# Optimization experiments

Measured on AMD Instinct MI355X. Metric: run time of the kernel, lower is better.

The kernel has to match this reference:

```python
import jax, jax.numpy as jnp
import numpy as np

B, N, C = 16, 4096, 512
PW, PH = 64, 64  # N = PW * PH
POOL = 2         # attention_pool_scale
D_SCALE = 1.0 / float(np.sqrt(C))


def setup_inputs() -> dict:
    key = jax.random.key(0)
    ks = jax.random.split(key, 4)
    w_std = 1.0 / float(np.sqrt(C))
    return {
        "x": jax.random.normal(ks[0], (B, N, C), dtype=jnp.float32),
        "Wq": jax.random.normal(ks[1], (C, C), dtype=jnp.float32) * w_std,
        "bq": jnp.zeros((C,), dtype=jnp.float32),
        "Wk": jax.random.normal(ks[2], (C, C), dtype=jnp.float32) * w_std,
        "bk": jnp.zeros((C,), dtype=jnp.float32),
        "Wv": jax.random.normal(ks[3], (C, C), dtype=jnp.float32) * w_std,
        "bv": jnp.zeros((C,), dtype=jnp.float32),
    }


def _to_spatial(t):
    # [B, N, C] -> [B, C, PW, PH]
    return t.transpose(0, 2, 1).reshape(t.shape[0], C, PW, PH)


def reference(x, Wq, bq, Wk, bk, Wv, bv):
    # Linear (torch convention y = x @ W^T + b) + sigmoid activation
    def proj(W, b):
        return jax.nn.sigmoid(jnp.einsum('bnc,dc->bnd', x, W) + b)

    Q = _to_spatial(proj(Wq, bq))  # [B, C, PW, PH]
    K = _to_spatial(proj(Wk, bk))
    V = _to_spatial(proj(Wv, bv))

    # avg_pool2d with kernel (POOL, 1): pool over PW axis
    q = Q.reshape(B, C, PW // POOL, POOL, PH).mean(axis=3)  # [B, C, PW/2, PH]
    k = K.reshape(B, C, PW // POOL, POOL, PH).mean(axis=3)

    # Qk = softmax(scale * Q @ k^T): [B, C, PW, PW/2]
    Qk = jax.nn.softmax(D_SCALE * jnp.einsum('bcik,bcjk->bcij', Q, k), axis=-1)
    # Kq = softmax(scale * q @ K^T): [B, C, PW/2, PW]
    Kq = jax.nn.softmax(D_SCALE * jnp.einsum('bcik,bcjk->bcij', q, K), axis=-1)
    # Kqv = Kq @ V: [B, C, PW/2, PH]
    Kqv = jnp.einsum('bcij,bcjk->bcik', Kq, V)
    # out = Qk @ Kqv: [B, C, PW, PH]
    out = jnp.einsum('bcij,bcjk->bcik', Qk, Kqv)

    # spatial -> sequence: [B, C, PW*PH] -> [B, N, C]
    return out.reshape(B, C, N).transpose(0, 2, 1)
```

## Files before the change

kernel.cpp:

```cpp
#include <hip/hip_runtime.h>
#include <hip/hip_bf16.h>
#include <string.h>

typedef __hip_bfloat16  bf16;
typedef __hip_bfloat162 bf162;
typedef __attribute__((ext_vector_type(8))) short short8;
typedef __attribute__((ext_vector_type(4))) float f32x4;

#define NB 16
#define NN 4096
#define NC 512
#define SCALE 0.044194173824159216f

#define GLL16(gp, lp) __builtin_amdgcn_global_load_lds( \
    (__attribute__((address_space(1))) void*)(gp),      \
    (__attribute__((address_space(3))) void*)(lp), 16, 0, 0)

__global__ __launch_bounds__(256) void cast_x_kernel(
    const float* __restrict__ x, bf16* __restrict__ xb)
{
    size_t i = ((size_t)blockIdx.x * 256 + threadIdx.x) * 8;
    float4 a = *(const float4*)(x + i);
    float4 b = *(const float4*)(x + i + 4);
    bf16 t[8];
    t[0] = __float2bfloat16(a.x); t[1] = __float2bfloat16(a.y);
    t[2] = __float2bfloat16(a.z); t[3] = __float2bfloat16(a.w);
    t[4] = __float2bfloat16(b.x); t[5] = __float2bfloat16(b.y);
    t[6] = __float2bfloat16(b.z); t[7] = __float2bfloat16(b.w);
    uint4 r; memcpy(&r, t, 16);
    *(uint4*)(xb + i) = r;
}

__global__ __launch_bounds__(256) void cast_w_kernel(
    const float* __restrict__ Wq, const float* __restrict__ Wk,
    const float* __restrict__ Wv, bf16* __restrict__ Wb)
{
    const float* W = (blockIdx.y == 0) ? Wq : (blockIdx.y == 1) ? Wk : Wv;
    size_t i = ((size_t)blockIdx.x * 256 + threadIdx.x) * 8;
    float4 a = *(const float4*)(W + i);
    float4 b = *(const float4*)(W + i + 4);
    bf16 t[8];
    t[0] = __float2bfloat16(a.x); t[1] = __float2bfloat16(a.y);
    t[2] = __float2bfloat16(a.z); t[3] = __float2bfloat16(a.w);
    t[4] = __float2bfloat16(b.x); t[5] = __float2bfloat16(b.y);
    t[6] = __float2bfloat16(b.z); t[7] = __float2bfloat16(b.w);
    uint4 r; memcpy(&r, t, 16);
    *(uint4*)(Wb + (size_t)blockIdx.y * (NC * NC) + i) = r;
}

__global__ __launch_bounds__(256) void proj_mfma(
    const bf16* __restrict__ xb, const bf16* __restrict__ Wb,
    const float* __restrict__ bq, const float* __restrict__ bk,
    const float* __restrict__ bv,
    bf16* __restrict__ Qs, bf16* __restrict__ Ks, bf16* __restrict__ Vs)
{
    __shared__ __align__(16) char smem[36864];
    short* As = (short*)smem;
    short* Bs = (short*)(smem + 16384);
    bf16*  OutS = (bf16*)smem;

    const int tid = threadIdx.x;
    const int w   = tid >> 6;
    const int l   = tid & 63;
    const int q   = l >> 4;
    const int mrow= l & 15;
    const int wr  = w >> 1;
    const int wc  = w & 1;

    const int bx = blockIdx.x;
    const int m  = bx >> 2;
    const int d0 = (bx & 3) * 128;
    const int r0 = blockIdx.y * 128;
    const int b  = r0 >> 12;
    const int n0 = r0 & 4095;

    const bf16*  W    = Wb + (size_t)m * (NC * NC);
    const float* bias = (m == 0) ? bq : (m == 1) ? bk : bv;
    bf16*        Out  = (m == 0) ? Qs : (m == 1) ? Ks : Vs;

    f32x4 acc[4][4];
    const f32x4 z = {0.f, 0.f, 0.f, 0.f};
    #pragma unroll
    for (int i = 0; i < 4; ++i)
        #pragma unroll
        for (int j = 0; j < 4; ++j) acc[i][j] = z;

    const int srow = tid >> 3;
    const int scol = (tid & 7) * 8;
    const int sxor = ((tid ^ (tid >> 3)) & 7) * 8;
    const int axor = (mrow & 7) * 8;

    for (int k0 = 0; k0 < NC; k0 += 64) {
        #pragma unroll
        for (int c = 0; c < 4; ++c) {
            int row = srow + 32 * c;
            GLL16(xb + (size_t)(r0 + row) * NC + k0 + sxor, &As[row * 64 + scol]);
        }
        #pragma unroll
        for (int c = 0; c < 4; ++c) {
            int row = srow + 32 * c;
            GLL16(W + (size_t)(d0 + row) * NC + k0 + sxor, &Bs[row * 64 + scol]);
        }
        __syncthreads();

        #pragma unroll
        for (int ks = 0; ks < 2; ++ks) {
            short8 af[4], bfr[4];
            #pragma unroll
            for (int ti = 0; ti < 4; ++ti)
                af[ti] = *(const short8*)&As[(64 * wr + 16 * ti + mrow) * 64 +
                                             ((q * 8 + 32 * ks) ^ axor)];
            #pragma unroll
            for (int tj = 0; tj < 4; ++tj)
                bfr[tj] = *(const short8*)&Bs[(64 * wc + 16 * tj + mrow) * 64 +
                                              ((q * 8 + 32 * ks) ^ axor)];
            #pragma unroll
            for (int ti = 0; ti < 4; ++ti)
                #pragma unroll
                for (int tj = 0; tj < 4; ++tj)
                    acc[ti][tj] = __builtin_amdgcn_mfma_f32_16x16x32_bf16(
                        af[ti], bfr[tj], acc[ti][tj], 0, 0, 0);
        }
        __syncthreads();
    }

    float bb[4];
    #pragma unroll
    for (int tj = 0; tj < 4; ++tj) bb[tj] = bias[d0 + 64 * wc + 16 * tj + mrow];

    #pragma unroll
    for (int ti = 0; ti < 4; ++ti)
        #pragma unroll
        for (int tj = 0; tj < 4; ++tj) {
            int d = 64 * wc + 16 * tj + mrow;
            bf16 t4[4];
            #pragma unroll
            for (int g = 0; g < 4; ++g) {
                float v = acc[ti][tj][g] + bb[tj];
                t4[g] = __float2bfloat16(1.0f / (1.0f + __expf(-v)));
            }
            uint2 pk; memcpy(&pk, t4, 8);
            *(uint2*)&OutS[d * 144 + 64 * wr + 16 * ti + 4 * q] = pk;
        }
    __syncthreads();

    #pragma unroll
    for (int v = 0; v < 8; ++v) {
        int e  = tid + 256 * v;
        int d  = e >> 4;
        int ch = e & 15;
        uint4 r = *(const uint4*)&OutS[d * 144 + ch * 8];
        *(uint4*)(Out + ((size_t)b * NC + d0 + d) * NN + n0 + ch * 8) = r;
    }
}

__global__ __launch_bounds__(256) void attn_mfma(
    const bf16* __restrict__ Qs, const bf16* __restrict__ Ks,
    const bf16* __restrict__ Vs, bf16* __restrict__ Os)
{
    __shared__ __align__(16) char smem[24064];
    bf16* VT  = (bf16*)smem;
    bf16* S1b = (bf16*)(smem + 9216);
    bf16* S2b = (bf16*)(smem + 9216 + 5120);
    bf16* KVT = (bf16*)(smem + 9216 + 5120 + 4608);

    const int tid = threadIdx.x;
    const int w   = tid >> 6;
    const int l   = tid & 63;
    const int m   = l & 15;
    const int q   = l >> 4;
    const size_t base = (size_t)blockIdx.x * NN;

    uint4  vr[2];
    short8 aQ[2];
    short8 bK8[8];
    {
        const uint4* src = (const uint4*)(Vs + base);
        vr[0] = src[tid];
        vr[1] = src[tid + 256];
        #pragma unroll
        for (int ks = 0; ks < 2; ++ks)
            aQ[ks] = *(const short8*)(Qs + base + (16 * w + m) * 64 + q * 8 + 32 * ks);
        #pragma unroll
        for (int tj = 0; tj < 4; ++tj)
            #pragma unroll
            for (int ks = 0; ks < 2; ++ks)
                bK8[tj * 2 + ks] = *(const short8*)(Ks + base + (16 * tj + m) * 64 + q * 8 + 32 * ks);
    }

    {
        #pragma unroll
        for (int v = 0; v < 2; ++v) {
            int e = tid + 256 * v;
            bf16 tmp[8]; memcpy(tmp, &vr[v], 16);
            int pw = e >> 3;
            int a  = e & 7;
            int cs = (((pw >> 3) ^ a) & 7) << 3;
            int c7 = pw & 7;
            #pragma unroll
            for (int t = 0; t < 8; ++t)
                VT[(8 * a + t) * 72 + cs + c7] = tmp[t];
        }
    }

    f32x4 tacc[4];
    {
        const f32x4 z = {0.f, 0.f, 0.f, 0.f};
        __builtin_amdgcn_s_setprio(1);
        #pragma unroll
        for (int tj = 0; tj < 4; ++tj) {
            tacc[tj] = z;
            #pragma unroll
            for (int ks = 0; ks < 2; ++ks)
                tacc[tj] = __builtin_amdgcn_mfma_f32_16x16x32_bf16(
                    aQ[ks], bK8[tj * 2 + ks], tacc[tj], 0, 0, 0);
        }
        __builtin_amdgcn_s_setprio(0);
    }

    {
        float e[4][4], s[4] = {0.f, 0.f, 0.f, 0.f};
        #pragma unroll
        for (int t = 0; t < 4; ++t)
            #pragma unroll
            for (int r = 0; r < 4; ++r) {
                float v  = tacc[t][r];
                float pv = (v + __shfl_xor(v, 1)) * (0.5f * SCALE);
                e[t][r] = __expf(pv);
                s[r] += e[t][r];
            }
        #pragma unroll
        for (int r = 0; r < 4; ++r) {
            #pragma unroll
            for (int d = 1; d < 16; d <<= 1)
                s[r] += __shfl_xor(s[r], d);
            s[r] = 2.0f / s[r];
        }
        {
            int jc = m >> 1;
            int t0 = (l & 1) * 2;
            #pragma unroll
            for (int tt = 0; tt < 2; ++tt) {
                int t = t0 + tt;
                #pragma unroll
                for (int r = 0; r < 4; ++r)
                    S1b[(16 * w + q * 4 + r) * 40 + t * 8 + jc] =
                        __float2bfloat16(e[t][r] * s[r]);
            }
        }
    }

    {
        float e2[4][2], s2[2] = {0.f, 0.f};
        #pragma unroll
        for (int t = 0; t < 4; ++t)
            #pragma unroll
            for (int h = 0; h < 2; ++h) {
                float pv = (tacc[t][2 * h] + tacc[t][2 * h + 1]) * (0.5f * SCALE);
                e2[t][h] = __expf(pv);
                s2[h] += e2[t][h];
            }
        #pragma unroll
        for (int h = 0; h < 2; ++h) {
            #pragma unroll
            for (int d = 1; d < 16; d <<= 1)
                s2[h] += __shfl_xor(s2[h], d);
            s2[h] = 1.0f / s2[h];
        }
        #pragma unroll
        for (int t = 0; t < 4; ++t)
            #pragma unroll
            for (int h = 0; h < 2; ++h)
                S2b[(8 * w + q * 2 + h) * 72 + t * 16 + m] =
                    __float2bfloat16(e2[t][h] * s2[h]);
    }
    __syncthreads();

    {
        const int rb = (2 * w + (m >> 3)) & 7;
        short8 aV[2];
        #pragma unroll
        for (int ks = 0; ks < 2; ++ks)
            aV[ks] = *(const short8*)&VT[(16 * w + m) * 72 +
                                         (((q + 4 * ks) ^ rb) & 7) * 8];
        __builtin_amdgcn_s_setprio(1);
        #pragma unroll
        for (int tn = 0; tn < 2; ++tn) {
            f32x4 kacc = {0.f, 0.f, 0.f, 0.f};
            #pragma unroll
            for (int ks = 0; ks < 2; ++ks) {
                short8 bS = *(const short8*)&S2b[(16 * tn + m) * 72 + q * 8 + 32 * ks];
                kacc = __builtin_amdgcn_mfma_f32_16x16x32_bf16(bS, aV[ks], kacc, 0, 0, 0);
            }
            bf16 t4[4];
            #pragma unroll
            for (int r = 0; r < 4; ++r) t4[r] = __float2bfloat16(kacc[r]);
            uint2 pk; memcpy(&pk, t4, 8);
            *(uint2*)&KVT[(16 * w + m) * 40 + 16 * tn + 4 * q] = pk;
        }
        __builtin_amdgcn_s_setprio(0);
    }
    __syncthreads();

    {
        short8 aS = *(const short8*)&S1b[(16 * w + m) * 40 + q * 8];
        __builtin_amdgcn_s_setprio(1);
        #pragma unroll
        for (int tn = 0; tn < 4; ++tn) {
            short8 bKV = *(const short8*)&KVT[(16 * tn + m) * 40 + q * 8];
            f32x4 z = {0.f, 0.f, 0.f, 0.f};
            f32x4 oacc = __builtin_amdgcn_mfma_f32_16x16x32_bf16(aS, bKV, z, 0, 0, 0);
            bf16 t4[4];
            #pragma unroll
            for (int r = 0; r < 4; ++r) t4[r] = __float2bfloat16(oacc[r]);
            uint2 pk; memcpy(&pk, t4, 8);
            *(uint2*)(Os + base + (size_t)(16 * tn + m) * 64 + 16 * w + 4 * q) = pk;
        }
        __builtin_amdgcn_s_setprio(0);
    }
}

__global__ __launch_bounds__(256) void unspat_kernel(
    const bf16* __restrict__ Os, float* __restrict__ out)
{
    __shared__ float t[32][65];
    const int b  = blockIdx.z;
    const int c0 = blockIdx.y * 32;
    const int bx = blockIdx.x;
    const int a0 = bx * 64;
    const int tx = threadIdx.x & 31;
    const int ty = threadIdx.x >> 5;
    const bf162* src = (const bf162*)(Os + ((size_t)b * NC + c0) * NN + a0);
    #pragma unroll
    for (int r = 0; r < 4; ++r) {
        int cc = ty + r * 8;
        float2 f = __bfloat1622float2(src[(size_t)cc * (NN/2) + tx]);
        t[cc][2*tx] = f.x; t[cc][2*tx+1] = f.y;
    }
    __syncthreads();
    float* dstB = out + ((size_t)b * NN) * NC + c0;
    #pragma unroll
    for (int r = 0; r < 8; ++r) {
        int nn = ty + r * 8;
        dstB[(size_t)(nn * 64 + bx) * NC + tx] = t[tx][nn];
    }
}

extern "C" void kernel_launch(void* const* d_in, const int* in_sizes, int n_in,
                              void* d_out, int out_size, void* d_ws, size_t ws_size,
                              hipStream_t stream)
{
    const float* x  = (const float*)d_in[0];
    const float* Wq = (const float*)d_in[1];
    const float* bq = (const float*)d_in[2];
    const float* Wk = (const float*)d_in[3];
    const float* bk = (const float*)d_in[4];
    const float* Wv = (const float*)d_in[5];
    const float* bv = (const float*)d_in[6];
    float* out = (float*)d_out;

    const size_t S = (size_t)NB * NC * NN;
    bf16* Qb = (bf16*)d_ws;
    bf16* Kb = Qb + S;
    bf16* Vb = Kb + S;
    bf16* xb = (bf16*)d_out;
    bf16* Wb = ((bf16*)d_out) + S;

    cast_x_kernel<<<dim3((NB * NN * NC) / (256 * 8)), 256, 0, stream>>>(x, xb);
    cast_w_kernel<<<dim3((NC * NC) / (256 * 8), 3), 256, 0, stream>>>(Wq, Wk, Wv, Wb);
    proj_mfma<<<dim3(12, (NB * NN) / 128), 256, 0, stream>>>(
        xb, Wb, bq, bk, bv, Qb, Kb, Vb);
    attn_mfma<<<dim3(NB * NC), 256, 0, stream>>>(Qb, Kb, Vb, Qb);
    unspat_kernel<<<dim3(NN / 64, NC / 32, NB), 256, 0, stream>>>(Qb, out);
}
```

Measured before the change: 497.0 us.

## Remap projection grid for XCD-aware L2 reuse and load K fragments lazily in attention

The projection kernel now runs on a 1D grid and remaps each workgroup index so that consecutive groups on the same XCD (index mod 8) share the same 128-row x tile across all 12 weight/column slices. This is meant to improve L2 reuse of x and W on MI355X, whose chiplets have separate L2 caches. In the attention kernel, the K fragments are no longer preloaded into a register array and are instead loaded just before each MFMA. That lowers register pressure but can expose load latency right before the matrix ops.

```diff
diff --git a/kernel.cpp b/kernel.cpp
--- a/kernel.cpp
+++ b/kernel.cpp
@@ -67,10 +67,13 @@
     const int wr  = w >> 1;
     const int wc  = w & 1;
 
-    const int bx = blockIdx.x;
-    const int m  = bx >> 2;
-    const int d0 = (bx & 3) * 128;
-    const int r0 = blockIdx.y * 128;
+    const int wg = blockIdx.x;
+    const int i  = wg >> 3;
+    const int s  = i % 12;
+    const int r  = (wg & 7) * 64 + i / 12;
+    const int m  = s >> 2;
+    const int d0 = (s & 3) * 128;
+    const int r0 = r * 128;
     const int b  = r0 >> 12;
     const int n0 = r0 & 4095;
 
@@ -81,9 +84,9 @@
     f32x4 acc[4][4];
     const f32x4 z = {0.f, 0.f, 0.f, 0.f};
     #pragma unroll
-    for (int i = 0; i < 4; ++i)
-        #pragma unroll
-        for (int j = 0; j < 4; ++j) acc[i][j] = z;
+    for (int ii = 0; ii < 4; ++ii)
+        #pragma unroll
+        for (int j = 0; j < 4; ++j) acc[ii][j] = z;
 
     const int srow = tid >> 3;
     const int scol = (tid & 7) * 8;
@@ -149,8 +152,8 @@
         int e  = tid + 256 * v;
         int d  = e >> 4;
         int ch = e & 15;
-        uint4 r = *(const uint4*)&OutS[d * 144 + ch * 8];
-        *(uint4*)(Out + ((size_t)b * NC + d0 + d) * NN + n0 + ch * 8) = r;
+        uint4 rr = *(const uint4*)&OutS[d * 144 + ch * 8];
+        *(uint4*)(Out + ((size_t)b * NC + d0 + d) * NN + n0 + ch * 8) = rr;
     }
 }
 
@@ -173,7 +176,6 @@
 
     uint4  vr[2];
     short8 aQ[2];
-    short8 bK8[8];
     {
         const uint4* src = (const uint4*)(Vs + base);
         vr[0] = src[tid];
@@ -181,11 +183,6 @@
         #pragma unroll
         for (int ks = 0; ks < 2; ++ks)
             aQ[ks] = *(const short8*)(Qs + base + (16 * w + m) * 64 + q * 8 + 32 * ks);
-        #pragma unroll
-        for (int tj = 0; tj < 4; ++tj)
-            #pragma unroll
-            for (int ks = 0; ks < 2; ++ks)
-                bK8[tj * 2 + ks] = *(const short8*)(Ks + base + (16 * tj + m) * 64 + q * 8 + 32 * ks);
     }
 
     {
@@ -211,9 +208,10 @@
         for (int tj = 0; tj < 4; ++tj) {
             tacc[tj] = z;
             #pragma unroll
-            for (int ks = 0; ks < 2; ++ks)
-                tacc[tj] = __builtin_amdgcn_mfma_f32_16x16x32_bf16(
-                    aQ[ks], bK8[tj * 2 + ks], tacc[tj], 0, 0, 0);
+            for (int ks = 0; ks < 2; ++ks) {
+                short8 bK = *(const short8*)(Ks + base + (16 * tj + m) * 64 + q * 8 + 32 * ks);
+                tacc[tj] = __builtin_amdgcn_mfma_f32_16x16x32_bf16(aQ[ks], bK, tacc[tj], 0, 0, 0);
+            }
         }
         __builtin_amdgcn_s_setprio(0);
     }
@@ -368,7 +366,7 @@
 
     cast_x_kernel<<<dim3((NB * NN * NC) / (256 * 8)), 256, 0, stream>>>(x, xb);
     cast_w_kernel<<<dim3((NC * NC) / (256 * 8), 3), 256, 0, stream>>>(Wq, Wk, Wv, Wb);
-    proj_mfma<<<dim3(12, (NB * NN) / 128), 256, 0, stream>>>(
+    proj_mfma<<<dim3(12 * (NB * NN) / 128), 256, 0, stream>>>(
         xb, Wb, bq, bk, bv, Qb, Kb, Vb);
     attn_mfma<<<dim3(NB * NC), 256, 0, stream>>>(Qb, Kb, Vb, Qb);
     unspat_kernel<<<dim3(NN / 64, NC / 32, NB), 256, 0, stream>>>(Qb, out);
```

After: 518.5 us. 1.04x slower.
